# Optimization experiments

Measured on AMD Instinct MI355X. Metric: run time of the kernel, lower is better.

## Reference

```python
import jax, jax.numpy as jnp
import numpy as np

B, S, H = 128, 1000, 256


def setup_inputs() -> dict:
    key = jax.random.key(0)
    ks = jax.random.split(key, 15)
    sc = 1.0 / np.sqrt(H)
    f = lambda k, shape: (jax.random.normal(k, shape, jnp.float32) * sc)
    return dict(
        static_hidden=jax.random.normal(ks[0], (B, S, H), jnp.float32),
        state_embedding=jax.random.normal(ks[1], (B, 1, H), jnp.float32),
        decoder_hidden=jax.random.normal(ks[2], (B, 1, H), jnp.float32),
        target_hidden=jax.random.normal(ks[3], (B, 1, H), jnp.float32),
        last_hh=jax.random.normal(ks[4], (1, B, H), jnp.float32),
        W_ih=f(ks[5], (3 * H, H)),
        W_hh=f(ks[6], (3 * H, H)),
        b_ih=f(ks[7], (3 * H,)),
        b_hh=f(ks[8], (3 * H,)),
        v_attn_enc=f(ks[9], (H,)),
        W_attn_enc=f(ks[10], (H, 2 * H)),
        v_attn_tgt=f(ks[11], (H,)),
        W_attn_tgt=f(ks[12], (H, 2 * H)),
        v_ptr=f(ks[13], (H,)),
        W_ptr=f(ks[14], (H, 3 * H)),
    )


def _attention(static, dec, v, W):
    # static: [B,S,H], dec: [B,1,H] -> softmax attention over S
    hid = jnp.concatenate([static, jnp.broadcast_to(dec, static.shape)], axis=2)  # [B,S,2H]
    t = jnp.tanh(jnp.einsum('hk,bsk->bhs', W, hid))  # [B,H,S]
    return jax.nn.softmax(jnp.einsum('h,bhs->bs', v, t), axis=1)  # [B,S]


def _gru_step(x, h, Wih, Whh, bih, bhh):
    # single-layer single-step torch GRU semantics; x,h: [B,H]
    gi = x @ Wih.T + bih
    gh = h @ Whh.T + bhh
    ir, iz, ig = jnp.split(gi, 3, axis=-1)
    hr, hz, hg = jnp.split(gh, 3, axis=-1)
    r = jax.nn.sigmoid(ir + hr)
    z = jax.nn.sigmoid(iz + hz)
    n = jnp.tanh(ig + r * hg)
    return (1.0 - z) * n + z * h


def _pointer_branch(static, state_emb, attn, v, W):
    context = jnp.einsum('bs,bsh->bh', attn, static)[:, None, :]  # [B,1,H]
    energy = jnp.concatenate(
        [static,
         jnp.broadcast_to(context, static.shape),
         jnp.broadcast_to(state_emb, static.shape)], axis=2)  # [B,S,3H]
    return jnp.einsum('h,bhs->bs', v, jnp.tanh(jnp.einsum('hk,bsk->bhs', W, energy)))


def reference(static_hidden, state_embedding, decoder_hidden, target_hidden, last_hh,
              W_ih, W_hh, b_ih, b_hh,
              v_attn_enc, W_attn_enc, v_attn_tgt, W_attn_tgt, v_ptr, W_ptr):
    # GRU step (dropout is identity in eval / p=0.0)
    h_new = _gru_step(decoder_hidden[:, 0, :], last_hh[0], W_ih, W_hh, b_ih, b_hh)
    rnn_out = h_new[:, None, :]  # [B,1,H]
    last_hh_new = h_new[None]    # [1,B,H]

    enc_attn = _attention(static_hidden, rnn_out, v_attn_enc, W_attn_enc)
    probs = _pointer_branch(static_hidden, state_embedding, enc_attn, v_ptr, W_ptr)

    tgt_attn = _attention(static_hidden, target_hidden, v_attn_tgt, W_attn_tgt)
    # NOTE: original code reuses self.v / self.W (not v_target/W_taret) for the
    # target branch energy -- replicated faithfully.
    probs_target = _pointer_branch(static_hidden, state_embedding, tgt_attn, v_ptr, W_ptr)

    return (5.0 * probs + probs_target, last_hh_new)
```

## Files before the change

### kernel.cpp

```cpp
#include <hip/hip_runtime.h>
#include <hip/hip_bf16.h>
#include <stdint.h>
#include <stddef.h>

#define Bn 128
#define Sn 1000
#define SP 1024
#define Hn 256

typedef __bf16 bf16;
typedef __bf16 bf16x8 __attribute__((ext_vector_type(8)));
typedef __bf16 bf16x4 __attribute__((ext_vector_type(4)));
typedef float  f32x16 __attribute__((ext_vector_type(16)));

__device__ __forceinline__ float fast_tanh(float x){
  return 1.0f - 2.0f / (__expf(2.0f * x) + 1.0f);
}
__device__ __forceinline__ float fast_sigmoid(float x){
  return 1.0f / (1.0f + __expf(-x));
}

__global__ void k0w(const float* __restrict__ We, const float* __restrict__ Wt,
                    const float* __restrict__ Wp, bf16* __restrict__ W2,
                    const float* __restrict__ dec, const float* __restrict__ lhh,
                    const float* __restrict__ tgt, const float* __restrict__ se,
                    float* __restrict__ xT, float* __restrict__ hT,
                    float* __restrict__ tT, float* __restrict__ sT){
  int blk = blockIdx.x, t = threadIdx.x;
  if (blk < 768){
    int tt = blk*256 + t;
    int e   = tt & 7;
    int l31 = (tt>>3) & 31;
    int lh2 = (tt>>8) & 1;
    int ks  = (tt>>9) & 1;
    int c   = (tt>>10) & 1;
    int kt  = (tt>>11) & 7;
    int hb  = tt >> 14;
    int r = (hb>>2)*256 + (hb&3)*64 + c*32 + l31;
    int k = kt*32 + ks*16 + lh2*8 + e;
    float val;
    if (r < 256)       val = We[r*512 + k];
    else if (r < 512)  val = Wt[(r-256)*512 + k];
    else               val = Wp[(r-512)*768 + k];
    W2[tt] = (bf16)val;
  } else {
    int idx = blk - 768;
    int a = idx >> 7, bb = idx & 127;
    const float* src = (a==0) ? dec : (a==1) ? lhh : (a==2) ? tgt : se;
    float* dst       = (a==0) ? xT  : (a==1) ? hT  : (a==2) ? tT  : sT;
    dst[t*128 + bb] = src[bb*256 + t];
  }
}

__global__ __launch_bounds__(512) void k1a_gru(
    const float* __restrict__ xT, const float* __restrict__ hT,
    const float* __restrict__ Wih, const float* __restrict__ Whh,
    const float* __restrict__ bih, const float* __restrict__ bhh,
    float* __restrict__ out_hh, float* __restrict__ hnT){
  int t = threadIdx.x;
  int g = t >> 7, b = t & 127;
  int h = blockIdx.x*4 + g;
  const float4* wir = (const float4*)(Wih + (size_t)h*256);
  const float4* wiz = (const float4*)(Wih + (size_t)(256+h)*256);
  const float4* wig = (const float4*)(Wih + (size_t)(512+h)*256);
  const float4* whr = (const float4*)(Whh + (size_t)h*256);
  const float4* whz = (const float4*)(Whh + (size_t)(256+h)*256);
  const float4* whg = (const float4*)(Whh + (size_t)(512+h)*256);
  float air=0.f, aiz=0.f, aig=0.f, ahr=0.f, ahz=0.f, ahg=0.f;
  #pragma unroll 2
  for (int kq=0; kq<64; kq++){
    float4 vir = wir[kq], viz = wiz[kq], vig = wig[kq];
    float4 vhr = whr[kq], vhz = whz[kq], vhg = whg[kq];
    #pragma unroll
    for (int e=0;e<4;e++){
      int k = kq*4 + e;
      float xv = xT[k*128 + b];
      float hv = hT[k*128 + b];
      air += (&vir.x)[e]*xv; aiz += (&viz.x)[e]*xv; aig += (&vig.x)[e]*xv;
      ahr += (&vhr.x)[e]*hv; ahz += (&vhz.x)[e]*hv; ahg += (&vhg.x)[e]*hv;
    }
  }
  air += bih[h];      ahr += bhh[h];
  aiz += bih[256+h];  ahz += bhh[256+h];
  aig += bih[512+h];  ahg += bhh[512+h];
  float r = fast_sigmoid(air + ahr);
  float z = fast_sigmoid(aiz + ahz);
  float n = fast_tanh(aig + r*ahg);
  float hprev = hT[h*128 + b];
  float hnew = (1.f - z)*n + z*hprev;
  out_hh[b*256 + h] = hnew;
  hnT[h*128 + b] = hnew;
}

__global__ __launch_bounds__(512) void k1c_dots(
    const float* __restrict__ hnT, const float* __restrict__ tT,
    const float* __restrict__ sT,
    const float* __restrict__ We, const float* __restrict__ Wt,
    const float* __restrict__ Wp,
    float* __restrict__ dEnc, float* __restrict__ dTgt, float* __restrict__ c3){
  int t = threadIdx.x;
  int g = t >> 7, b = t & 127;
  int vr = blockIdx.x*4 + g;
  int var = vr >> 8, h = vr & 255;
  const float* wrow; const float* X; float* dst;
  if (var == 0)      { wrow = We + (size_t)h*512 + 256; X = hnT; dst = dEnc; }
  else if (var == 1) { wrow = Wt + (size_t)h*512 + 256; X = tT;  dst = dTgt; }
  else               { wrow = Wp + (size_t)h*768 + 512; X = sT;  dst = c3; }
  const float4* w4 = (const float4*)wrow;
  float acc = 0.f;
  #pragma unroll 2
  for (int kq=0; kq<64; kq++){
    float4 wv = w4[kq];
    #pragma unroll
    for (int e=0;e<4;e++)
      acc += (&wv.x)[e] * X[(kq*4+e)*128 + b];
  }
  dst[b*256 + h] = acc;
}

__global__ __launch_bounds__(256, 2) void k2_gemm(
    const float* __restrict__ stat, const bf16* __restrict__ W2,
    const float* __restrict__ dEnc, const float* __restrict__ dTgt,
    const float* __restrict__ vEnc, const float* __restrict__ vTgt,
    float* __restrict__ scE, float* __restrict__ scT, bf16* __restrict__ Aptr){
  __shared__ __align__(16) bf16 As[64*256];
  __shared__ float scr[2][4][64];
  int tid = threadIdx.x, w = tid>>6, l = tid&63;
  int l31 = l&31, lh = l>>5;
  int st = blockIdx.x, b = blockIdx.y;

  {
    int am = tid>>2, agk = tid&3;
    bool aValid = (st*64 + am) < Sn;
    const float4* aSrc4 = (const float4*)(stat + ((size_t)b*Sn + st*64 + am)*Hn);
    #pragma unroll
    for (int i=0;i<8;i++){
      int G = i*4 + agk;
      float4 f0 = make_float4(0.f,0.f,0.f,0.f), f1 = f0;
      if (aValid){ f0 = aSrc4[G*2]; f1 = aSrc4[G*2+1]; }
      bf16x8 v;
      v[0]=(bf16)f0.x; v[1]=(bf16)f0.y; v[2]=(bf16)f0.z; v[3]=(bf16)f0.w;
      v[4]=(bf16)f1.x; v[5]=(bf16)f1.y; v[6]=(bf16)f1.z; v[7]=(bf16)f1.w;
      *(bf16x8*)&As[am*256 + ((G ^ (am&7))<<3)] = v;
    }
  }
  __syncthreads();

#define WLOAD(dst, it) { \
  const bf16* wp_ = W2 + ((size_t)(((it)>>3)*4 + w)*8 + (size_t)((it)&7))*2048 + l*8; \
  dst[0] = *(const bf16x8*)(wp_); \
  dst[1] = *(const bf16x8*)(wp_ + 512); \
  dst[2] = *(const bf16x8*)(wp_ + 1024); \
  dst[3] = *(const bf16x8*)(wp_ + 1536); }

#define CHUNK(it, wf) { \
  _Pragma("unroll") \
  for (int ks=0; ks<2; ks++){ \
    int G_ = ((it)&7)*4 + ks*2 + lh; \
    int sa_ = (G_ ^ (l31&7))<<3; \
    bf16x8 af0 = *(const bf16x8*)&As[l31*256 + sa_]; \
    bf16x8 af1 = *(const bf16x8*)&As[(32+l31)*256 + sa_]; \
    acc[0][0] = __builtin_amdgcn_mfma_f32_32x32x16_bf16(wf[ks],   af0, acc[0][0], 0,0,0); \
    acc[1][0] = __builtin_amdgcn_mfma_f32_32x32x16_bf16(wf[ks],   af1, acc[1][0], 0,0,0); \
    acc[0][1] = __builtin_amdgcn_mfma_f32_32x32x16_bf16(wf[2+ks], af0, acc[0][1], 0,0,0); \
    acc[1][1] = __builtin_amdgcn_mfma_f32_32x32x16_bf16(wf[2+ks], af1, acc[1][1], 0,0,0); \
  } }

  bf16x8 wA[4], wB[4];
  WLOAD(wA, 0);
  WLOAD(wB, 1);

  float scp0[2] = {0.f,0.f}, scp1[2] = {0.f,0.f};
  f32x16 acc[2][2];

  #pragma unroll
  for (int p=0; p<3; p++){
    #pragma unroll
    for (int a=0;a<2;a++)
      #pragma unroll
      for (int c=0;c<2;c++)
        #pragma unroll
        for (int r=0;r<16;r++) acc[a][c][r] = 0.f;

    #pragma unroll
    for (int kq=0; kq<4; kq++){
      int it = p*8 + kq*2;
      CHUNK(it, wA);
      if (it+2 < 24) WLOAD(wA, it+2);
      CHUNK(it+1, wB);
      if (it+3 < 24) WLOAD(wB, it+3);
    }

    if (p < 2){
      const float* vv = p ? vTgt : vEnc;
      const float* db = (p ? dTgt : dEnc) + b*256;
      float s0 = 0.f, s1 = 0.f;
      #pragma unroll
      for (int c=0;c<2;c++){
        int nb = w*64 + c*32 + 4*lh;
        #pragma unroll
        for (int r=0;r<16;r++){
          int n = nb + (r&3) + 8*(r>>2);
          float vdv = vv[n], ddv = db[n];
          s0 += vdv * fast_tanh(acc[0][c][r] + ddv);
          s1 += vdv * fast_tanh(acc[1][c][r] + ddv);
        }
      }
      scp0[p] = s0; scp1[p] = s1;
    }
  }

  __syncthreads();
  #pragma unroll
  for (int a=0;a<2;a++){
    int m = a*32 + l31;
    #pragma unroll
    for (int c=0;c<2;c++){
      int g0 = w*8 + c*4 + lh*2;
      bf16x8 lo, hi;
      #pragma unroll
      for (int r=0;r<8;r++){ lo[r] = (bf16)acc[a][c][r]; hi[r] = (bf16)acc[a][c][8+r]; }
      *(bf16x8*)&As[m*256 + (( g0    ^ (m&7))<<3)] = lo;
      *(bf16x8*)&As[m*256 + (((g0+1) ^ (m&7))<<3)] = hi;
    }
  }
  #pragma unroll
  for (int p2=0;p2<2;p2++){
    float v0 = scp0[p2] + __shfl_xor(scp0[p2], 32);
    float v1 = scp1[p2] + __shfl_xor(scp1[p2], 32);
    if (lh == 0){
      scr[p2][w][l31]      = v0;
      scr[p2][w][32 + l31] = v1;
    }
  }
  __syncthreads();
  if (tid < 128){
    int pp = tid>>6, m = tid&63;
    float s = scr[pp][0][m] + scr[pp][1][m] + scr[pp][2][m] + scr[pp][3][m];
    (pp ? scT : scE)[b*SP + st*64 + m] = s;
  }
  {
    int m = tid>>2, part = tid&3;
    bf16* dst = Aptr + ((size_t)(b*1024 + st*64 + m))*256 + part*64;
    #pragma unroll
    for (int i=0;i<8;i++){
      int g = (part*8 + i) ^ (m&7);
      *(bf16x8*)(dst + i*8) = *(const bf16x8*)&As[m*256 + (g<<3)];
    }
  }
#undef WLOAD
#undef CHUNK
}

__global__ __launch_bounds__(1024) void k3_ctx(
    const float* __restrict__ scE, const float* __restrict__ scT,
    const float* __restrict__ stat, float* __restrict__ ctxG){
  __shared__ float attE[500], attT[500];
  __shared__ float redE[16], redT[16];
  __shared__ float4 pe4[16][64], pt4[16][64];
  int b = blockIdx.x, sg = blockIdx.y, t = threadIdx.x;
  int wid = t>>6, ln = t&63;

  float vE = (t < Sn) ? scE[b*SP + t] : -1e30f;
  float vT = (t < Sn) ? scT[b*SP + t] : -1e30f;
  float mE = vE, mT = vT;
  #pragma unroll
  for (int o=1;o<64;o<<=1){ mE=fmaxf(mE,__shfl_xor(mE,o)); mT=fmaxf(mT,__shfl_xor(mT,o)); }
  if (ln==0){ redE[wid]=mE; redT[wid]=mT; }
  __syncthreads();
  float ME=-1e30f, MT=-1e30f;
  #pragma unroll
  for (int i=0;i<16;i++){ ME=fmaxf(ME,redE[i]); MT=fmaxf(MT,redT[i]); }
  __syncthreads();
  float eE = (t < Sn) ? __expf(vE-ME) : 0.f;
  float eT = (t < Sn) ? __expf(vT-MT) : 0.f;
  float sE=eE, sT=eT;
  #pragma unroll
  for (int o=1;o<64;o<<=1){ sE+=__shfl_xor(sE,o); sT+=__shfl_xor(sT,o); }
  if (ln==0){ redE[wid]=sE; redT[wid]=sT; }
  __syncthreads();
  float SE=0.f, ST=0.f;
  #pragma unroll
  for (int i=0;i<16;i++){ SE+=redE[i]; ST+=redT[i]; }
  float invE = 1.f/SE, invT = 1.f/ST;
  if (t < 500){
    int s = sg*500 + t;
    attE[t] = __expf(scE[b*SP+s]-ME)*invE;
    attT[t] = __expf(scT[b*SP+s]-MT)*invT;
  }
  __syncthreads();

  int h4 = t & 63, rg = t >> 6;
  float4 aE = make_float4(0.f,0.f,0.f,0.f), aT = aE;
  int nrows = (rg == 15) ? 20 : 32;
  const float4* base = (const float4*)(stat + ((size_t)(b*Sn + sg*500 + rg*32))*Hn) + h4;
  #pragma unroll 4
  for (int i=0;i<nrows;i++){
    float4 f = base[(size_t)i*64];
    float wE = attE[rg*32 + i], wT = attT[rg*32 + i];
    aE.x += wE*f.x; aE.y += wE*f.y; aE.z += wE*f.z; aE.w += wE*f.w;
    aT.x += wT*f.x; aT.y += wT*f.y; aT.z += wT*f.z; aT.w += wT*f.w;
  }
  pe4[rg][h4] = aE; pt4[rg][h4] = aT;
  __syncthreads();
  if (t < 64){
    float4 s = make_float4(0.f,0.f,0.f,0.f);
    #pragma unroll
    for (int i=0;i<16;i++){
      float4 p = pe4[i][t];
      s.x+=p.x; s.y+=p.y; s.z+=p.z; s.w+=p.w;
    }
    atomicAdd(&ctxG[b*256 + t*4 + 0], s.x);
    atomicAdd(&ctxG[b*256 + t*4 + 1], s.y);
    atomicAdd(&ctxG[b*256 + t*4 + 2], s.z);
    atomicAdd(&ctxG[b*256 + t*4 + 3], s.w);
  } else if (t < 128){
    int h = t - 64;
    float4 s = make_float4(0.f,0.f,0.f,0.f);
    #pragma unroll
    for (int i=0;i<16;i++){
      float4 p = pt4[i][h];
      s.x+=p.x; s.y+=p.y; s.z+=p.z; s.w+=p.w;
    }
    atomicAdd(&ctxG[32768 + b*256 + h*4 + 0], s.x);
    atomicAdd(&ctxG[32768 + b*256 + h*4 + 1], s.y);
    atomicAdd(&ctxG[32768 + b*256 + h*4 + 2], s.z);
    atomicAdd(&ctxG[32768 + b*256 + h*4 + 3], s.w);
  }
}

__global__ __launch_bounds__(512) void k3c_c2(
    const float* __restrict__ ctxG, const float* __restrict__ Wp,
    const float* __restrict__ c3,
    float* __restrict__ cE, float* __restrict__ cT){
  __shared__ __align__(16) float ctxL[512];
  int b = blockIdx.x, t = threadIdx.x;
  ctxL[t] = ctxG[(t>>8)*32768 + b*256 + (t&255)];
  __syncthreads();
  int var = t >> 8, h = t & 255;
  const float4* w4 = (const float4*)(Wp + (size_t)h*768 + 256);
  const float4* cv = (const float4*)(&ctxL[var*256]);
  float acc = 0.f;
  #pragma unroll 4
  for (int k=0;k<64;k++){
    float4 wv = w4[k], xv = cv[k];
    acc += wv.x*xv.x + wv.y*xv.y + wv.z*xv.z + wv.w*xv.w;
  }
  (var ? cT : cE)[b*256 + h] = acc + c3[b*256 + h];
}

__global__ __launch_bounds__(256) void k4_final(
    const bf16* __restrict__ Aptr, const float* __restrict__ cE,
    const float* __restrict__ cT, const float* __restrict__ vp,
    float* __restrict__ out){
  int t = threadIdx.x;
  int st = blockIdx.x, b = blockIdx.y;
  int m = t>>2, part = t&3;
  const bf16* src = Aptr + ((size_t)(b*1024 + st*64 + m))*256 + part*64;
  const float* vpb = vp + part*64;
  const float* ceb = cE + b*256 + part*64;
  const float* ctb = cT + b*256 + part*64;
  float pe = 0.f, pt = 0.f;
  #pragma unroll
  for (int i=0;i<8;i++){
    bf16x8 av = *(const bf16x8*)(src + i*8);
    int bi = ((i>>2)<<5) + (((i>>1)&1)<<2) + ((i&1)<<4);
    float4 v0 = *(const float4*)(vpb + bi), v1 = *(const float4*)(vpb + bi + 8);
    float4 e0 = *(const float4*)(ceb + bi), e1 = *(const float4*)(ceb + bi + 8);
    float4 t0 = *(const float4*)(ctb + bi), t1 = *(const float4*)(ctb + bi + 8);
    #pragma unroll
    for (int j=0;j<4;j++){
      float a = (float)av[j];
      pe += (&v0.x)[j] * fast_tanh(a + (&e0.x)[j]);
      pt += (&v0.x)[j] * fast_tanh(a + (&t0.x)[j]);
    }
    #pragma unroll
    for (int j=0;j<4;j++){
      float a = (float)av[4+j];
      pe += (&v1.x)[j] * fast_tanh(a + (&e1.x)[j]);
      pt += (&v1.x)[j] * fast_tanh(a + (&t1.x)[j]);
    }
  }
  pe += __shfl_xor(pe,1); pe += __shfl_xor(pe,2);
  pt += __shfl_xor(pt,1); pt += __shfl_xor(pt,2);
  int s = st*64 + m;
  if (part==0 && s < Sn) out[(size_t)b*Sn + s] = 5.0f*pe + pt;
}

extern "C" void kernel_launch(void* const* d_in, const int* in_sizes, int n_in,
                              void* d_out, int out_size, void* d_ws, size_t ws_size,
                              hipStream_t stream){
  const float* stat = (const float*)d_in[0];
  const float* se   = (const float*)d_in[1];
  const float* dec  = (const float*)d_in[2];
  const float* tgt  = (const float*)d_in[3];
  const float* lhh  = (const float*)d_in[4];
  const float* Wih  = (const float*)d_in[5];
  const float* Whh  = (const float*)d_in[6];
  const float* bih  = (const float*)d_in[7];
  const float* bhh  = (const float*)d_in[8];
  const float* vEnc = (const float*)d_in[9];
  const float* WEnc = (const float*)d_in[10];
  const float* vTgt = (const float*)d_in[11];
  const float* WTgt = (const float*)d_in[12];
  const float* vPtr = (const float*)d_in[13];
  const float* WPtr = (const float*)d_in[14];
  float* out = (float*)d_out;

  char* wsp = (char*)d_ws;
  bf16*  Aptr = (bf16*)(wsp);
  bf16*  W2   = (bf16*)(wsp + 67108864);
  float* xT   = (float*)(wsp + 67502080);
  float* hT   = (float*)(wsp + 67633152);
  float* tT   = (float*)(wsp + 67764224);
  float* sT   = (float*)(wsp + 67895296);
  float* hnT  = (float*)(wsp + 68026368);
  float* scE  = (float*)(wsp + 68157440);
  float* scT  = (float*)(wsp + 68681728);
  float* dEnc = (float*)(wsp + 69206016);
  float* dTgt = (float*)(wsp + 69337088);
  float* c3   = (float*)(wsp + 69468160);
  float* cE   = (float*)(wsp + 69599232);
  float* cT   = (float*)(wsp + 69730304);
  float* ctxG = (float*)(wsp + 69861376);

  hipMemsetAsync(ctxG, 0, 262144, stream);
  hipLaunchKernelGGL(k0w, dim3(1280), dim3(256), 0, stream,
                     WEnc, WTgt, WPtr, W2, dec, lhh, tgt, se, xT, hT, tT, sT);
  hipLaunchKernelGGL(k1a_gru, dim3(64), dim3(512), 0, stream,
                     xT, hT, Wih, Whh, bih, bhh, out + Bn*Sn, hnT);
  hipLaunchKernelGGL(k1c_dots, dim3(192), dim3(512), 0, stream,
                     hnT, tT, sT, WEnc, WTgt, WPtr, dEnc, dTgt, c3);
  hipLaunchKernelGGL(k2_gemm, dim3(16, 128), dim3(256), 0, stream,
                     stat, W2, dEnc, dTgt, vEnc, vTgt, scE, scT, Aptr);
  hipLaunchKernelGGL(k3_ctx, dim3(128, 2), dim3(1024), 0, stream,
                     scE, scT, stat, ctxG);
  hipLaunchKernelGGL(k3c_c2, dim3(128), dim3(512), 0, stream,
                     ctxG, WPtr, c3, cE, cT);
  hipLaunchKernelGGL(k4_final, dim3(16, 128), dim3(256), 0, stream,
                     Aptr, cE, cT, vPtr, out);
}
```

Baseline: 519.3 us.

## Stage weight tiles into LDS via direct global-to-LDS double-buffered loads

The bf16 weight matrix is now stored in plain row-major layout instead of a pre-swizzled per-lane MFMA layout. The GEMM kernel double-buffers 256x32 weight tiles into shared memory with global_load_lds, using an XOR swizzle, and reads MFMA B fragments from LDS. Manual waitcnt and s_barrier calls pipeline the copy of chunk it+2 with compute on chunk it. This frees the VGPRs that held register-prefetched weight fragments, but adds 32KB of LDS per block and two barriers per k-chunk, which may reduce occupancy or stall.

```diff
diff --git a/kernel.cpp b/kernel.cpp
--- a/kernel.cpp
+++ b/kernel.cpp
@@ -13,6 +13,9 @@
 typedef __bf16 bf16x4 __attribute__((ext_vector_type(4)));
 typedef float  f32x16 __attribute__((ext_vector_type(16)));
 
+typedef __attribute__((address_space(1))) const unsigned int* gas1;
+typedef __attribute__((address_space(3))) unsigned int* las3;
+
 __device__ __forceinline__ float fast_tanh(float x){
   return 1.0f - 2.0f / (__expf(2.0f * x) + 1.0f);
 }
@@ -21,7 +24,7 @@
 }
 
 __global__ void k0w(const float* __restrict__ We, const float* __restrict__ Wt,
-                    const float* __restrict__ Wp, bf16* __restrict__ W2,
+                    const float* __restrict__ Wp, bf16* __restrict__ Wcb,
                     const float* __restrict__ dec, const float* __restrict__ lhh,
                     const float* __restrict__ tgt, const float* __restrict__ se,
                     float* __restrict__ xT, float* __restrict__ hT,
@@ -29,20 +32,12 @@
   int blk = blockIdx.x, t = threadIdx.x;
   if (blk < 768){
     int tt = blk*256 + t;
-    int e   = tt & 7;
-    int l31 = (tt>>3) & 31;
-    int lh2 = (tt>>8) & 1;
-    int ks  = (tt>>9) & 1;
-    int c   = (tt>>10) & 1;
-    int kt  = (tt>>11) & 7;
-    int hb  = tt >> 14;
-    int r = (hb>>2)*256 + (hb&3)*64 + c*32 + l31;
-    int k = kt*32 + ks*16 + lh2*8 + e;
+    int r = tt >> 8, c = tt & 255;
     float val;
-    if (r < 256)       val = We[r*512 + k];
-    else if (r < 512)  val = Wt[(r-256)*512 + k];
-    else               val = Wp[(r-512)*768 + k];
-    W2[tt] = (bf16)val;
+    if (r < 256)       val = We[r*512 + c];
+    else if (r < 512)  val = Wt[(r-256)*512 + c];
+    else               val = Wp[(r-512)*768 + c];
+    Wcb[tt] = (bf16)val;
   } else {
     int idx = blk - 768;
     int a = idx >> 7, bb = idx & 127;
@@ -119,15 +114,19 @@
 }
 
 __global__ __launch_bounds__(256, 2) void k2_gemm(
-    const float* __restrict__ stat, const bf16* __restrict__ W2,
+    const float* __restrict__ stat, const bf16* __restrict__ Wcb,
     const float* __restrict__ dEnc, const float* __restrict__ dTgt,
     const float* __restrict__ vEnc, const float* __restrict__ vTgt,
     float* __restrict__ scE, float* __restrict__ scT, bf16* __restrict__ Aptr){
   __shared__ __align__(16) bf16 As[64*256];
+  __shared__ __align__(16) bf16 Bs[2][256*32];
   __shared__ float scr[2][4][64];
   int tid = threadIdx.x, w = tid>>6, l = tid&63;
   int l31 = l&31, lh = l>>5;
   int st = blockIdx.x, b = blockIdx.y;
+
+  int bnb = w*16 + (l>>2);
+  int bg  = l&3;
 
   {
     int am = tid>>2, agk = tid&3;
@@ -146,29 +145,41 @@
   }
   __syncthreads();
 
-#define WLOAD(dst, it) { \
-  const bf16* wp_ = W2 + ((size_t)(((it)>>3)*4 + w)*8 + (size_t)((it)&7))*2048 + l*8; \
-  dst[0] = *(const bf16x8*)(wp_); \
-  dst[1] = *(const bf16x8*)(wp_ + 512); \
-  dst[2] = *(const bf16x8*)(wp_ + 1024); \
-  dst[3] = *(const bf16x8*)(wp_ + 1536); }
-
-#define CHUNK(it, wf) { \
+#define STAGE(it, buf) { \
+  const bf16* wb_ = Wcb + (size_t)((it)>>3)*65536 + ((it)&7)*32; \
+  _Pragma("unroll") \
+  for (int i_=0;i_<4;i_++){ \
+    int n_ = i_*64 + bnb; \
+    int g_ = bg ^ ((n_>>1)&3); \
+    __builtin_amdgcn_global_load_lds((gas1)(wb_ + (size_t)n_*256 + g_*8), \
+        (las3)(&Bs[buf][i_*2048 + w*512]), 16, 0, 0); \
+  } }
+
+#define CHUNK(it) { \
+  const bf16* bsr_ = &Bs[(it)&1][0]; \
   _Pragma("unroll") \
   for (int ks=0; ks<2; ks++){ \
-    int G_ = ((it)&7)*4 + ks*2 + lh; \
+    int kg_ = ks*2 + lh; \
+    int G_ = ((it)&7)*4 + kg_; \
     int sa_ = (G_ ^ (l31&7))<<3; \
     bf16x8 af0 = *(const bf16x8*)&As[l31*256 + sa_]; \
     bf16x8 af1 = *(const bf16x8*)&As[(32+l31)*256 + sa_]; \
-    acc[0][0] = __builtin_amdgcn_mfma_f32_32x32x16_bf16(wf[ks],   af0, acc[0][0], 0,0,0); \
-    acc[1][0] = __builtin_amdgcn_mfma_f32_32x32x16_bf16(wf[ks],   af1, acc[1][0], 0,0,0); \
-    acc[0][1] = __builtin_amdgcn_mfma_f32_32x32x16_bf16(wf[2+ks], af0, acc[0][1], 0,0,0); \
-    acc[1][1] = __builtin_amdgcn_mfma_f32_32x32x16_bf16(wf[2+ks], af1, acc[1][1], 0,0,0); \
+    _Pragma("unroll") \
+    for (int c_=0;c_<2;c_++){ \
+      int n_ = w*64 + c_*32 + l31; \
+      bf16x8 wf = *(const bf16x8*)&bsr_[n_*32 + ((kg_ ^ ((n_>>1)&3))<<3)]; \
+      acc[0][c_] = __builtin_amdgcn_mfma_f32_32x32x16_bf16(wf, af0, acc[0][c_], 0,0,0); \
+      acc[1][c_] = __builtin_amdgcn_mfma_f32_32x32x16_bf16(wf, af1, acc[1][c_], 0,0,0); \
+    } \
   } }
 
-  bf16x8 wA[4], wB[4];
-  WLOAD(wA, 0);
-  WLOAD(wB, 1);
+  STAGE(0, 0);
+  STAGE(1, 1);
+  __builtin_amdgcn_sched_barrier(0);
+  asm volatile("s_waitcnt vmcnt(4)" ::: "memory");
+  __builtin_amdgcn_sched_barrier(0);
+  __builtin_amdgcn_s_barrier();
+  __builtin_amdgcn_sched_barrier(0);
 
   float scp0[2] = {0.f,0.f}, scp1[2] = {0.f,0.f};
   f32x16 acc[2][2];
@@ -183,12 +194,21 @@
         for (int r=0;r<16;r++) acc[a][c][r] = 0.f;
 
     #pragma unroll
-    for (int kq=0; kq<4; kq++){
-      int it = p*8 + kq*2;
-      CHUNK(it, wA);
-      if (it+2 < 24) WLOAD(wA, it+2);
-      CHUNK(it+1, wB);
-      if (it+3 < 24) WLOAD(wB, it+3);
+    for (int kt=0; kt<8; kt++){
+      int it = p*8 + kt;
+      CHUNK(it);
+      if (it < 23){
+        __builtin_amdgcn_sched_barrier(0);
+        __builtin_amdgcn_s_barrier();
+        __builtin_amdgcn_sched_barrier(0);
+        if (it < 22){ STAGE(it+2, (it&1)); }
+        __builtin_amdgcn_sched_barrier(0);
+        if (it < 22){ asm volatile("s_waitcnt vmcnt(4)" ::: "memory"); }
+        else        { asm volatile("s_waitcnt vmcnt(0)" ::: "memory"); }
+        __builtin_amdgcn_sched_barrier(0);
+        __builtin_amdgcn_s_barrier();
+        __builtin_amdgcn_sched_barrier(0);
+      }
     }
 
     if (p < 2){
@@ -248,7 +268,7 @@
       *(bf16x8*)(dst + i*8) = *(const bf16x8*)&As[m*256 + (g<<3)];
     }
   }
-#undef WLOAD
+#undef STAGE
 #undef CHUNK
 }
 
@@ -409,7 +429,7 @@
 
   char* wsp = (char*)d_ws;
   bf16*  Aptr = (bf16*)(wsp);
-  bf16*  W2   = (bf16*)(wsp + 67108864);
+  bf16*  Wcb  = (bf16*)(wsp + 67108864);
   float* xT   = (float*)(wsp + 67502080);
   float* hT   = (float*)(wsp + 67633152);
   float* tT   = (float*)(wsp + 67764224);
@@ -426,13 +446,13 @@
 
   hipMemsetAsync(ctxG, 0, 262144, stream);
   hipLaunchKernelGGL(k0w, dim3(1280), dim3(256), 0, stream,
-                     WEnc, WTgt, WPtr, W2, dec, lhh, tgt, se, xT, hT, tT, sT);
+                     WEnc, WTgt, WPtr, Wcb, dec, lhh, tgt, se, xT, hT, tT, sT);
   hipLaunchKernelGGL(k1a_gru, dim3(64), dim3(512), 0, stream,
                      xT, hT, Wih, Whh, bih, bhh, out + Bn*Sn, hnT);
   hipLaunchKernelGGL(k1c_dots, dim3(192), dim3(512), 0, stream,
                      hnT, tT, sT, WEnc, WTgt, WPtr, dEnc, dTgt, c3);
   hipLaunchKernelGGL(k2_gemm, dim3(16, 128), dim3(256), 0, stream,
-                     stat, W2, dEnc, dTgt, vEnc, vTgt, scE, scT, Aptr);
+                     stat, Wcb, dEnc, dTgt, vEnc, vTgt, scE, scT, Aptr);
   hipLaunchKernelGGL(k3_ctx, dim3(128, 2), dim3(1024), 0, stream,
                      scE, scT, stat, ctxG);
   hipLaunchKernelGGL(k3c_c2, dim3(128), dim3(512), 0, stream,
```

Result: faster. 455.2 us (-12.3%).
